# Kernel tuning notes

Hardware: AMD Instinct MI355X
Metric: run time of the kernel (lower is better)

Reference implementation:

```python
import jax, jax.numpy as jnp
import numpy as np
import math

B, T, D = 2, 2048, 1024
H, NL, DF = 16, 6, 4096
HD = D // H
EPS = 1e-5

def layer_norm(x, w, b):
    mu = jnp.mean(x, axis=-1, keepdims=True)
    var = jnp.mean((x - mu) ** 2, axis=-1, keepdims=True)
    return (x - mu) * jax.lax.rsqrt(var + EPS) * w + b

def setup_inputs() -> dict:
    key = jax.random.key(0)
    ks = jax.random.split(key, 12)
    def w(k, shape, scale=0.02):
        return jax.random.normal(k, shape, dtype=jnp.float32) * scale
    inp = {
        'sequences': jax.random.normal(ks[0], (B, T, D), dtype=jnp.float32),
        'Wq': w(ks[1], (NL, D, D)), 'bq': jnp.zeros((NL, D), jnp.float32),
        'Wk': w(ks[2], (NL, D, D)), 'bk': jnp.zeros((NL, D), jnp.float32),
        'Wv': w(ks[3], (NL, D, D)), 'bv': jnp.zeros((NL, D), jnp.float32),
        'Wo': w(ks[4], (NL, D, D)), 'bo': jnp.zeros((NL, D), jnp.float32),
        'Wz': w(ks[5], (NL, D, D)), 'bz': jnp.zeros((NL, D), jnp.float32),
        'Wr': w(ks[6], (NL, D, D)), 'br': jnp.zeros((NL, D), jnp.float32),
        'W1': w(ks[7], (NL, D, DF)), 'b1': jnp.zeros((NL, DF), jnp.float32),
        'W2': w(ks[8], (NL, DF, D)), 'b2': jnp.zeros((NL, D), jnp.float32),
        'ln1_w': jnp.ones((NL, D), jnp.float32), 'ln1_b': jnp.zeros((NL, D), jnp.float32),
        'ln2_w': jnp.ones((NL, D), jnp.float32), 'ln2_b': jnp.zeros((NL, D), jnp.float32),
        'lnf_w': jnp.ones((D,), jnp.float32), 'lnf_b': jnp.zeros((D,), jnp.float32),
    }
    return inp

def reference(sequences, Wq, bq, Wk, bk, Wv, bv, Wo, bo, Wz, bz, Wr, br,
              W1, b1, W2, b2, ln1_w, ln1_b, ln2_w, ln2_b, lnf_w, lnf_b):
    scale = 1.0 / math.sqrt(HD)
    causal = jnp.tril(jnp.ones((T, T), dtype=bool))  # mask[L:L+T, :L+T] with L=0
    x = sequences
    src = x
    for i in range(NL):
        xn = layer_norm(x, ln1_w[i], ln1_b[i])
        # QKV -> [B, H, T, HD]
        q = (xn @ Wq[i] + bq[i]).reshape(B, T, H, HD).transpose(0, 2, 1, 3)
        k = (xn @ Wk[i] + bk[i]).reshape(B, T, H, HD).transpose(0, 2, 1, 3)
        v = (xn @ Wv[i] + bv[i]).reshape(B, T, H, HD).transpose(0, 2, 1, 3)
        att = jnp.einsum('bhqd,bhkd->bhqk', q, k) * scale
        att = jnp.where(causal, att, -jnp.inf)
        att = jax.nn.softmax(att, axis=-1)
        y = jnp.einsum('bhqk,bhkd->bhqd', att, v)
        y = y.transpose(0, 2, 1, 3).reshape(B, T, D)
        x_attn = y @ Wo[i] + bo[i]
        z = jax.nn.sigmoid(xn @ Wz[i] + bz[i])
        r = jax.nn.sigmoid(xn @ Wr[i] + br[i])
        h_tilde = jnp.tanh(r * x_attn)
        x = (1.0 - z) * x + z * h_tilde
        xm = layer_norm(x, ln2_w[i], ln2_b[i])
        mlp = jax.nn.gelu(xm @ W1[i] + b1[i], approximate=False) @ W2[i] + b2[i]
        x = (1.0 - z) * x + z * mlp
        x = x + src
    x = layer_norm(x, lnf_w, lnf_b)
    return x
```

## Files before the change

kernel.cpp:

```cpp
#include <hip/hip_runtime.h>
#include <hip/hip_bf16.h>
#include <math.h>

#define B_ 2
#define T_ 2048
#define D_ 1024
#define H_ 16
#define NL_ 6
#define DF_ 4096
#define HD_ 64
#define M_ (B_*T_)

typedef __bf16 bf16;
typedef __attribute__((ext_vector_type(8))) __bf16 bf16x8;
typedef __attribute__((ext_vector_type(4))) float f32x4;
typedef __attribute__((ext_vector_type(16))) float f32x16;
typedef __attribute__((ext_vector_type(4))) unsigned u32x4;

#define BAR() __builtin_amdgcn_s_barrier()
#define LGKM0() asm volatile("s_waitcnt lgkmcnt(0)" ::: "memory")
#define VMC(n) asm volatile("s_waitcnt vmcnt(" #n ")" ::: "memory")

__device__ __forceinline__ void gload_lds16(const void* g, void* l) {
    __builtin_amdgcn_global_load_lds((const __attribute__((address_space(1))) void*)g,
                                     (__attribute__((address_space(3))) void*)l, 16, 0, 0);
}

__device__ __forceinline__ unsigned pk2(float a, float b) {
    bf16 lo = (bf16)a, hb = (bf16)b;
    return (unsigned)__builtin_bit_cast(unsigned short, lo) |
           ((unsigned)__builtin_bit_cast(unsigned short, hb) << 16);
}

template<bool OUT_BF16>
__global__ __launch_bounds__(256) void ln_kernel(const float* __restrict__ x,
        const float* __restrict__ w, const float* __restrict__ b,
        void* __restrict__ out) {
    const int row = blockIdx.x;
    const int t = threadIdx.x;
    const float4 xv = *(const float4*)(x + (long)row * D_ + t * 4);
    float s  = xv.x + xv.y + xv.z + xv.w;
    float sq = xv.x*xv.x + xv.y*xv.y + xv.z*xv.z + xv.w*xv.w;
    #pragma unroll
    for (int m = 32; m; m >>= 1) { s += __shfl_xor(s, m); sq += __shfl_xor(sq, m); }
    __shared__ float red[8];
    const int wid = t >> 6, lid = t & 63;
    if (lid == 0) { red[wid] = s; red[wid + 4] = sq; }
    __syncthreads();
    s  = red[0] + red[1] + red[2] + red[3];
    sq = red[4] + red[5] + red[6] + red[7];
    const float mu   = s * (1.0f / D_);
    const float var  = sq * (1.0f / D_) - mu * mu;
    const float rstd = rsqrtf(var + 1e-5f);
    const float4 wv = *(const float4*)(w + t * 4);
    const float4 bv = *(const float4*)(b + t * 4);
    float o0 = (xv.x - mu) * rstd * wv.x + bv.x;
    float o1 = (xv.y - mu) * rstd * wv.y + bv.y;
    float o2 = (xv.z - mu) * rstd * wv.z + bv.z;
    float o3 = (xv.w - mu) * rstd * wv.w + bv.w;
    if (OUT_BF16) {
        bf16* o = (bf16*)out + (long)row * D_ + t * 4;
        o[0] = (bf16)o0; o[1] = (bf16)o1; o[2] = (bf16)o2; o[3] = (bf16)o3;
    } else {
        float* o = (float*)out + (long)row * D_ + t * 4;
        o[0] = o0; o[1] = o1; o[2] = o2; o[3] = o3;
    }
}

__global__ __launch_bounds__(256) void wconv_all(
        const float* __restrict__ Wq, const float* __restrict__ Wk,
        const float* __restrict__ Wv, const float* __restrict__ Wz,
        const float* __restrict__ Wr, const float* __restrict__ Wo,
        const float* __restrict__ W1, const float* __restrict__ W2,
        bf16* __restrict__ wt) {
    __shared__ float s[32][33];
    const int bid = blockIdx.x;
    const float* src; bf16* dst; int t, K, nlg;
    if (bid < 6144) {
        const int m = bid >> 10; t = bid & 1023; K = 1024; nlg = 5;
        switch (m) {
            case 0: src = Wq; dst = wt; break;
            case 1: src = Wk; dst = wt + (1u << 20); break;
            case 2: src = Wv; dst = wt + (2u << 20); break;
            case 3: src = Wz; dst = wt + (3u << 20); break;
            case 4: src = Wr; dst = wt + (4u << 20); break;
            default: src = Wo; dst = wt + (5u << 20); break;
        }
    } else if (bid < 10240) {
        t = bid - 6144; K = 1024; nlg = 7; src = W1; dst = wt + (6u << 20);
    } else {
        t = bid - 10240; K = 4096; nlg = 5; src = W2; dst = wt + (10u << 20);
    }
    const int N = 1 << (nlg + 5);
    const int k0 = (t >> nlg) * 32, n0 = (t & ((1 << nlg) - 1)) * 32;
    const int c = threadIdx.x & 31, r8 = threadIdx.x >> 5;
    #pragma unroll
    for (int it = 0; it < 4; it++)
        s[r8 + it*8][c] = src[(long)(k0 + r8 + it*8) * N + n0 + c];
    __syncthreads();
    #pragma unroll
    for (int it = 0; it < 4; it++)
        dst[(long)(n0 + r8 + it*8) * K + k0 + c] = (bf16)s[c][r8 + it*8];
}

#define MFMA16(a, b, c) __builtin_amdgcn_mfma_f32_16x16x32_bf16(a, b, c, 0, 0, 0)

__device__ __forceinline__ void gemm128_core(const bf16* __restrict__ A, const bf16* __restrict__ Bt,
        const int Ks, const int NT, const int m0, const int n0, char* lds, f32x4 (&acc)[4][4]) {
    const int tid = threadIdx.x;
    const int lane = tid & 63, w = tid >> 6;
    const int wm = w >> 1, wn = w & 1;
    const int cl = lane & 15, gl = lane >> 4;
    const int srow = lane >> 2;
    const int sxc = (((lane & 3) ^ (srow & 3)) << 3);
    const bf16* pa0 = A  + (size_t)(m0 + w * 32 + srow) * Ks + sxc;
    const bf16* pa1 = pa0 + (size_t)16 * Ks;
    const bf16* pb  = Bt + (size_t)(n0 + w * 16 + srow) * Ks + sxc;
    char* laA = lds + w * 2048;
    char* laB = lds + 32768 + w * 1024;

#define STG(KT, BUF) do { \
    gload_lds16(pa0 + (size_t)(KT) * 32, laA + (BUF) * 16384); \
    gload_lds16(pa1 + (size_t)(KT) * 32, laA + (BUF) * 16384 + 1024); \
    gload_lds16(pb  + (size_t)(KT) * 32, laB + (BUF) * 8192); } while (0)

    STG(0, 0); STG(1, 1);
    VMC(3);
    BAR();

    const int xo  = ((gl ^ (cl & 3)) << 4);
    const int rdA = (wm * 64 + cl) * 64 + xo;
    const int rdB = (wn * 64 + cl) * 64 + xo;

    for (int kt = 0; kt < NT; ++kt) {
        const int buf = kt & 1;
        const char* sA = lds + buf * 16384;
        const char* sB = lds + 32768 + buf * 8192;
        bf16x8 a[4], b[4];
        #pragma unroll
        for (int mi = 0; mi < 4; mi++) a[mi] = *(const bf16x8*)(sA + rdA + mi * 1024);
        #pragma unroll
        for (int ni = 0; ni < 4; ni++) b[ni] = *(const bf16x8*)(sB + rdB + ni * 1024);
        BAR(); LGKM0();
        __builtin_amdgcn_s_setprio(1);
        #pragma unroll
        for (int mi = 0; mi < 2; mi++)
            #pragma unroll
            for (int ni = 0; ni < 4; ni++)
                acc[mi][ni] = MFMA16(a[mi], b[ni], acc[mi][ni]);
        __builtin_amdgcn_s_setprio(0);
        BAR();
        if (kt + 2 < NT) STG(kt + 2, buf);
        __builtin_amdgcn_s_setprio(1);
        #pragma unroll
        for (int mi = 2; mi < 4; mi++)
            #pragma unroll
            for (int ni = 0; ni < 4; ni++)
                acc[mi][ni] = MFMA16(a[mi], b[ni], acc[mi][ni]);
        __builtin_amdgcn_s_setprio(0);
        if (kt + 2 < NT)      { VMC(3); }
        else if (kt + 1 < NT) { VMC(0); }
        BAR();
    }
#undef STG
}

__global__ __launch_bounds__(512, 4) void gemm5_k(const bf16* __restrict__ A, const bf16* __restrict__ Bt,
        const float* __restrict__ bq, const float* __restrict__ bk, const float* __restrict__ bvv,
        const float* __restrict__ bz, const float* __restrict__ br,
        bf16* __restrict__ oq, bf16* __restrict__ ok, bf16* __restrict__ ov,
        float* __restrict__ oz, float* __restrict__ orr) {
    __shared__ __align__(16) char lds[49152];
    int bid = blockIdx.x;
    bid = (bid & 7) * 80 + (bid >> 3);
    const int m0 = (bid / 40) * 256, n0 = (bid % 40) * 128;
    f32x4 acc[4][4];
    #pragma unroll
    for (int i = 0; i < 4; i++)
        #pragma unroll
        for (int j = 0; j < 4; j++) acc[i][j] = (f32x4){0.f, 0.f, 0.f, 0.f};
    gemm128_core(A, Bt, 1024, 32, m0, n0, lds, acc);
    const int tid = threadIdx.x, lane = tid & 63, w = tid >> 6;
    const int wm = w >> 1, wn = w & 1, cl = lane & 15, gl = lane >> 4;
    const int seg = n0 >> 10;
    const int lc0 = (n0 & 1023) + wn * 64;
    const float* bias; int mode; void* outp;
    switch (seg) {
        case 0:  bias = bq;  mode = 0; outp = oq;  break;
        case 1:  bias = bk;  mode = 0; outp = ok;  break;
        case 2:  bias = bvv; mode = 1; outp = ov;  break;
        case 3:  bias = bz;  mode = 2; outp = oz;  break;
        default: bias = br;  mode = 2; outp = orr; break;
    }
    #pragma unroll
    for (int mi = 0; mi < 4; mi++) {
        #pragma unroll
        for (int ni = 0; ni < 4; ni++) {
            const int lcol = lc0 + ni * 16 + cl;
            const float bv = bias[lcol];
            #pragma unroll
            for (int r = 0; r < 4; r++) {
                const int row = m0 + wm * 64 + mi * 16 + gl * 4 + r;
                const float v = acc[mi][ni][r] + bv;
                if (mode == 0) {
                    ((bf16*)outp)[(long)row * 1024 + lcol] = (bf16)v;
                } else if (mode == 1) {
                    ((bf16*)outp)[((long)(row >> 11) * 1024 + lcol) * T_ + (row & 2047)] = (bf16)v;
                } else {
                    ((float*)outp)[(long)row * 1024 + lcol] = 1.0f / (1.0f + __expf(-v));
                }
            }
        }
    }
}

__global__ __launch_bounds__(512, 4) void gemmG_k(const bf16* __restrict__ A, const bf16* __restrict__ Bt,
        const float* __restrict__ bias, bf16* __restrict__ out) {
    __shared__ __align__(16) char lds[49152];
    int bid = blockIdx.x;
    bid = (bid & 7) * 64 + (bid >> 3);
    const int m0 = (bid >> 5) * 256, n0 = (bid & 31) * 128;
    f32x4 acc[4][4];
    #pragma unroll
    for (int i = 0; i < 4; i++)
        #pragma unroll
        for (int j = 0; j < 4; j++) acc[i][j] = (f32x4){0.f, 0.f, 0.f, 0.f};
    gemm128_core(A, Bt, 1024, 32, m0, n0, lds, acc);
    const int tid = threadIdx.x, lane = tid & 63, w = tid >> 6;
    const int wm = w >> 1, wn = w & 1, cl = lane & 15, gl = lane >> 4;
    #pragma unroll
    for (int mi = 0; mi < 4; mi++) {
        #pragma unroll
        for (int ni = 0; ni < 4; ni++) {
            const int col = n0 + wn * 64 + ni * 16 + cl;
            const float bv = bias[col];
            #pragma unroll
            for (int r = 0; r < 4; r++) {
                const int row = m0 + wm * 64 + mi * 16 + gl * 4 + r;
                float v = acc[mi][ni][r] + bv;
                v = 0.5f * v * (1.0f + erff(v * 0.70710678118f));
                out[(long)row * DF_ + col] = (bf16)v;
            }
        }
    }
}

__global__ __launch_bounds__(512, 4) void gemmP_k(const bf16* __restrict__ A, const bf16* __restrict__ Bt,
        float* __restrict__ p0, float* __restrict__ p1, float* __restrict__ p2, float* __restrict__ p3) {
    __shared__ __align__(16) char lds[49152];
    int bid = blockIdx.x;
    bid = (bid & 7) * 64 + (bid >> 3);
    const int mt = bid >> 5, s = (bid >> 3) & 3, ntl = bid & 7;
    const int m0 = mt * 256, n0 = ntl * 128;
    f32x4 acc[4][4];
    #pragma unroll
    for (int i = 0; i < 4; i++)
        #pragma unroll
        for (int j = 0; j < 4; j++) acc[i][j] = (f32x4){0.f, 0.f, 0.f, 0.f};
    gemm128_core(A + s * 1024, Bt + s * 1024, 4096, 32, m0, n0, lds, acc);
    float* outp = (s == 0) ? p0 : (s == 1) ? p1 : (s == 2) ? p2 : p3;
    const int tid = threadIdx.x, lane = tid & 63, w = tid >> 6;
    const int wm = w >> 1, wn = w & 1, cl = lane & 15, gl = lane >> 4;
    #pragma unroll
    for (int mi = 0; mi < 4; mi++) {
        #pragma unroll
        for (int ni = 0; ni < 4; ni++) {
            const int col = n0 + wn * 64 + ni * 16 + cl;
            #pragma unroll
            for (int r = 0; r < 4; r++) {
                const int row = m0 + wm * 64 + mi * 16 + gl * 4 + r;
                outp[(long)row * 1024 + col] = acc[mi][ni][r];
            }
        }
    }
}

__global__ __launch_bounds__(256) void gemmWo_kernel(const bf16* __restrict__ A,
        const bf16* __restrict__ Bt, const float* __restrict__ bias,
        float* __restrict__ out) {
    __shared__ bf16 sA[128 * 32];
    __shared__ bf16 sB[128 * 32];
    const int tid = threadIdx.x;
    int bid = blockIdx.x;
    bid = (bid & 7) * 32 + (bid >> 3);
    const int m0 = (bid >> 3) * 128, n0 = (bid & 7) * 128;
    f32x4 acc[4][4];
    #pragma unroll
    for (int i = 0; i < 4; i++)
        #pragma unroll
        for (int j = 0; j < 4; j++) acc[i][j] = (f32x4){0.f, 0.f, 0.f, 0.f};
    const int lane = tid & 63, w = tid >> 6;
    const int wr = (w >> 1) * 64, wc = (w & 1) * 64;
    const int cl = lane & 15, gl = lane >> 4;
    const int srow = tid >> 2, skoff = (tid & 3) * 8;
    const bf16* ga = A  + (long)(m0 + srow) * D_ + skoff;
    const bf16* gb = Bt + (long)(n0 + srow) * D_ + skoff;
    char* sAc = (char*)sA;
    char* sBc = (char*)sB;
    const int wb = w * 1024;
    for (int k0 = 0; k0 < D_; k0 += 32) {
        if (k0) __syncthreads();
        gload_lds16(ga + k0,            sAc + wb);
        gload_lds16(ga + 64 * D_ + k0,  sAc + 4096 + wb);
        gload_lds16(gb + k0,            sBc + wb);
        gload_lds16(gb + 64 * D_ + k0,  sBc + 4096 + wb);
        __syncthreads();
        bf16x8 af[4], bfr[4];
        #pragma unroll
        for (int i = 0; i < 4; i++) af[i]  = *(const bf16x8*)(sA + (wr + i*16 + cl) * 32 + 8 * gl);
        #pragma unroll
        for (int j = 0; j < 4; j++) bfr[j] = *(const bf16x8*)(sB + (wc + j*16 + cl) * 32 + 8 * gl);
        #pragma unroll
        for (int i = 0; i < 4; i++)
            #pragma unroll
            for (int j = 0; j < 4; j++)
                acc[i][j] = MFMA16(af[i], bfr[j], acc[i][j]);
    }
    #pragma unroll
    for (int i = 0; i < 4; i++) {
        #pragma unroll
        for (int j = 0; j < 4; j++) {
            const int gcol = n0 + wc + j * 16 + cl;
            const float bv = bias[gcol];
            #pragma unroll
            for (int r = 0; r < 4; r++) {
                const int grow = m0 + wr + i * 16 + gl * 4 + r;
                out[(long)grow * D_ + gcol] = acc[i][j][r] + bv;
            }
        }
    }
}

#define LOADKV(K0,K1,K2,K3,V00,V01,V10,V11,KVB) do { \
    const long kro_ = (long)((KVB) + col) * D_ + 8 * hi; \
    K0 = *(const bf16x8*)(kB + kro_); \
    K1 = *(const bf16x8*)(kB + kro_ + 16); \
    K2 = *(const bf16x8*)(kB + kro_ + 32); \
    K3 = *(const bf16x8*)(kB + kro_ + 48); \
    const long vro_ = (long)col * T_ + (KVB) + 8 * hi; \
    V00 = *(const bf16x8*)(vB + vro_); \
    V10 = *(const bf16x8*)(vB + vro_ + 16); \
    V01 = *(const bf16x8*)(vB + vro_ + (long)32 * T_); \
    V11 = *(const bf16x8*)(vB + vro_ + (long)32 * T_ + 16); \
} while (0)

#define PROC(K0,K1,K2,K3,V00,V01,V10,V11,JJ) do { \
    f32x16 S; \
    _Pragma("unroll") for (int i_ = 0; i_ < 16; i_++) S[i_] = 0.f; \
    S = __builtin_amdgcn_mfma_f32_32x32x16_bf16(K0, qf0, S, 0, 0, 0); \
    S = __builtin_amdgcn_mfma_f32_32x32x16_bf16(K1, qf1, S, 0, 0, 0); \
    S = __builtin_amdgcn_mfma_f32_32x32x16_bf16(K2, qf2, S, 0, 0, 0); \
    S = __builtin_amdgcn_mfma_f32_32x32x16_bf16(K3, qf3, S, 0, 0, 0); \
    float p_[16]; \
    const bool dg_ = (JJ) == nt - 1; \
    _Pragma("unroll") for (int r_ = 0; r_ < 16; r_++) { \
        p_[r_] = S[r_] * 0.125f; \
        const int kvl_ = (r_ & 3) + 8 * (r_ >> 2) + 4 * hi; \
        if (dg_ && kvl_ > col) p_[r_] = -3.0e38f; \
    } \
    float tm_ = p_[0]; \
    _Pragma("unroll") for (int r_ = 1; r_ < 16; r_++) tm_ = fmaxf(tm_, p_[r_]); \
    tm_ = fmaxf(tm_, __shfl_xor(tm_, 32)); \
    const float mn_ = fmaxf(mrun, tm_); \
    const float al_ = __expf(mrun - mn_); \
    mrun = mn_; \
    float ts_ = 0.f; \
    _Pragma("unroll") for (int r_ = 0; r_ < 16; r_++) { p_[r_] = __expf(p_[r_] - mn_); ts_ += p_[r_]; } \
    ts_ += __shfl_xor(ts_, 32); \
    lrun = lrun * al_ + ts_; \
    _Pragma("unroll") for (int i_ = 0; i_ < 16; i_++) { Od0[i_] *= al_; Od1[i_] *= al_; } \
    const unsigned w0_ = pk2(p_[0],  p_[1]),  w1_ = pk2(p_[2],  p_[3]); \
    const unsigned w2_ = pk2(p_[4],  p_[5]),  w3_ = pk2(p_[6],  p_[7]); \
    const unsigned w4_ = pk2(p_[8],  p_[9]),  w5_ = pk2(p_[10], p_[11]); \
    const unsigned w6_ = pk2(p_[12], p_[13]), w7_ = pk2(p_[14], p_[15]); \
    const unsigned x0_ = __shfl_xor((int)w0_, 32), x1_ = __shfl_xor((int)w1_, 32); \
    const unsigned x2_ = __shfl_xor((int)w2_, 32), x3_ = __shfl_xor((int)w3_, 32); \
    const unsigned x4_ = __shfl_xor((int)w4_, 32), x5_ = __shfl_xor((int)w5_, 32); \
    const unsigned x6_ = __shfl_xor((int)w6_, 32), x7_ = __shfl_xor((int)w7_, 32); \
    const u32x4 c0_ = hi ? (u32x4){x2_, x3_, w2_, w3_} : (u32x4){w0_, w1_, x0_, x1_}; \
    const u32x4 c1_ = hi ? (u32x4){x6_, x7_, w6_, w7_} : (u32x4){w4_, w5_, x4_, x5_}; \
    const bf16x8 pb0_ = __builtin_bit_cast(bf16x8, c0_); \
    const bf16x8 pb1_ = __builtin_bit_cast(bf16x8, c1_); \
    Od0 = __builtin_amdgcn_mfma_f32_32x32x16_bf16(V00, pb0_, Od0, 0, 0, 0); \
    Od0 = __builtin_amdgcn_mfma_f32_32x32x16_bf16(V10, pb1_, Od0, 0, 0, 0); \
    Od1 = __builtin_amdgcn_mfma_f32_32x32x16_bf16(V01, pb0_, Od1, 0, 0, 0); \
    Od1 = __builtin_amdgcn_mfma_f32_32x32x16_bf16(V11, pb1_, Od1, 0, 0, 0); \
} while (0)

__global__ __launch_bounds__(128) void attn_kernel(const bf16* __restrict__ q,
        const bf16* __restrict__ k, const bf16* __restrict__ vT,
        bf16* __restrict__ y) {
    const int tid = threadIdx.x, wid = tid >> 6, lane = tid & 63;
    const int col = lane & 31, hi = lane >> 5;
    const int bid = blockIdx.x;
    const int xcd = bid & 7, idx = bid >> 3;
    const int bh = xcd + 8 * (idx & 3);
    const int g = idx >> 2;
    const int qt = wid ? (63 - g) : g;
    const int qb = qt * 32;
    const int b = bh >> 4, h = bh & 15;

    const bf16* qB = q  + (long)b * T_ * D_ + h * HD_;
    const bf16* kB = k  + (long)b * T_ * D_ + h * HD_;
    const bf16* vB = vT + (long)b * D_ * T_ + (long)h * HD_ * T_;

    bf16x8 qf0, qf1, qf2, qf3;
    {
        const long qo = (long)(qb + col) * D_ + 8 * hi;
        qf0 = *(const bf16x8*)(qB + qo);
        qf1 = *(const bf16x8*)(qB + qo + 16);
        qf2 = *(const bf16x8*)(qB + qo + 32);
        qf3 = *(const bf16x8*)(qB + qo + 48);
    }

    f32x16 Od0, Od1;
    #pragma unroll
    for (int i = 0; i < 16; i++) { Od0[i] = 0.f; Od1[i] = 0.f; }
    float mrun = -INFINITY, lrun = 0.f;

    bf16x8 ka0, ka1, ka2, ka3, va00, va01, va10, va11;
    bf16x8 kb0, kb1, kb2, kb3, vb00, vb01, vb10, vb11;
    const int nt = qt + 1;

    int jj = 0;
    LOADKV(ka0, ka1, ka2, ka3, va00, va01, va10, va11, 0);
    while (true) {
        if (jj + 1 < nt) LOADKV(kb0, kb1, kb2, kb3, vb00, vb01, vb10, vb11, (jj + 1) * 32);
        PROC(ka0, ka1, ka2, ka3, va00, va01, va10, va11, jj);
        if (++jj >= nt) break;
        if (jj + 1 < nt) LOADKV(ka0, ka1, ka2, ka3, va00, va01, va10, va11, (jj + 1) * 32);
        PROC(kb0, kb1, kb2, kb3, vb00, vb01, vb10, vb11, jj);
        if (++jj >= nt) break;
    }

    const float inv = 1.0f / lrun;
    bf16* yr = y + (long)(b * T_ + qb + col) * D_ + h * HD_;
    #pragma unroll
    for (int rg = 0; rg < 4; rg++) {
        const int d0 = 8 * rg + 4 * hi;
        uint2 s0 = { pk2(Od0[4*rg] * inv, Od0[4*rg+1] * inv), pk2(Od0[4*rg+2] * inv, Od0[4*rg+3] * inv) };
        *(uint2*)(yr + d0) = s0;
        uint2 s1 = { pk2(Od1[4*rg] * inv, Od1[4*rg+1] * inv), pk2(Od1[4*rg+2] * inv, Od1[4*rg+3] * inv) };
        *(uint2*)(yr + 32 + d0) = s1;
    }
}

__global__ __launch_bounds__(256) void gate1_kernel(float* __restrict__ x,
        const float* __restrict__ z, const float* __restrict__ r,
        const float* __restrict__ xa) {
    const long i = ((long)blockIdx.x * 256 + threadIdx.x) * 4;
    float4 xv = *(const float4*)(x + i);
    const float4 zv = *(const float4*)(z + i);
    const float4 rv = *(const float4*)(r + i);
    const float4 av = *(const float4*)(xa + i);
    xv.x = (1.f - zv.x) * xv.x + zv.x * tanhf(rv.x * av.x);
    xv.y = (1.f - zv.y) * xv.y + zv.y * tanhf(rv.y * av.y);
    xv.z = (1.f - zv.z) * xv.z + zv.z * tanhf(rv.z * av.z);
    xv.w = (1.f - zv.w) * xv.w + zv.w * tanhf(rv.w * av.w);
    *(float4*)(x + i) = xv;
}

__global__ __launch_bounds__(256) void gate2_kernel(float* __restrict__ x,
        const float* __restrict__ z,
        const float* __restrict__ p0, const float* __restrict__ p1,
        const float* __restrict__ p2, const float* __restrict__ p3,
        const float* __restrict__ src, const float* __restrict__ b2) {
    const long i = ((long)blockIdx.x * 256 + threadIdx.x) * 4;
    float4 xv = *(const float4*)(x + i);
    const float4 zv = *(const float4*)(z + i);
    const float4 a0 = *(const float4*)(p0 + i);
    const float4 a1 = *(const float4*)(p1 + i);
    const float4 a2 = *(const float4*)(p2 + i);
    const float4 a3 = *(const float4*)(p3 + i);
    const float4 sv = *(const float4*)(src + i);
    const float4 bb = *(const float4*)(b2 + (i & 1023));
    const float mx = a0.x + a1.x + a2.x + a3.x + bb.x;
    const float my = a0.y + a1.y + a2.y + a3.y + bb.y;
    const float mz = a0.z + a1.z + a2.z + a3.z + bb.z;
    const float mw = a0.w + a1.w + a2.w + a3.w + bb.w;
    xv.x = (1.f - zv.x) * xv.x + zv.x * mx + sv.x;
    xv.y = (1.f - zv.y) * xv.y + zv.y * my + sv.y;
    xv.z = (1.f - zv.z) * xv.z + zv.z * mz + sv.z;
    xv.w = (1.f - zv.w) * xv.w + zv.w * mw + sv.w;
    *(float4*)(x + i) = xv;
}

extern "C" void kernel_launch(void* const* d_in, const int* in_sizes, int n_in,
                              void* d_out, int out_size, void* d_ws, size_t ws_size,
                              hipStream_t stream) {
    const float* seq   = (const float*)d_in[0];
    const float* Wq    = (const float*)d_in[1];  const float* bq = (const float*)d_in[2];
    const float* Wk    = (const float*)d_in[3];  const float* bk = (const float*)d_in[4];
    const float* Wv    = (const float*)d_in[5];  const float* bv = (const float*)d_in[6];
    const float* Wo    = (const float*)d_in[7];  const float* bo = (const float*)d_in[8];
    const float* Wz    = (const float*)d_in[9];  const float* bz = (const float*)d_in[10];
    const float* Wr    = (const float*)d_in[11]; const float* br = (const float*)d_in[12];
    const float* W1    = (const float*)d_in[13]; const float* b1 = (const float*)d_in[14];
    const float* W2    = (const float*)d_in[15]; const float* b2 = (const float*)d_in[16];
    const float* ln1w  = (const float*)d_in[17]; const float* ln1b = (const float*)d_in[18];
    const float* ln2w  = (const float*)d_in[19]; const float* ln2b = (const float*)d_in[20];
    const float* lnfw  = (const float*)d_in[21]; const float* lnfb = (const float*)d_in[22];

    char* ws = (char*)d_ws;
    float* x   = (float*)(ws);
    float* z   = (float*)(ws + ((size_t)16 << 20));
    float* r   = (float*)(ws + ((size_t)32 << 20));
    float* xa  = (float*)(ws + ((size_t)48 << 20));
    bf16*  xn  = (bf16*)(ws + ((size_t)64 << 20));
    bf16*  qb_ = (bf16*)(ws + ((size_t)72 << 20));
    bf16*  kb_ = (bf16*)(ws + ((size_t)80 << 20));
    bf16*  vtb = (bf16*)(ws + ((size_t)88 << 20));
    bf16*  yb  = (bf16*)(ws + ((size_t)96 << 20));
    bf16*  h1  = (bf16*)(ws + ((size_t)104 << 20));
    bf16*  wt  = (bf16*)(ws + ((size_t)136 << 20));
    float* pt2 = (float*)(ws + ((size_t)172 << 20));
    float* pt3 = (float*)(ws + ((size_t)188 << 20));

    bf16* wto = wt + (5u << 20);
    bf16* wt1 = wt + (6u << 20);
    bf16* wt2 = wt + (10u << 20);

    hipMemcpyAsync(x, seq, (size_t)M_ * D_ * 4, hipMemcpyDeviceToDevice, stream);

    for (int i = 0; i < NL_; i++) {
        const long dd = (long)i * D_ * D_;
        wconv_all<<<14336, 256, 0, stream>>>(Wq + dd, Wk + dd, Wv + dd, Wz + dd,
                                             Wr + dd, Wo + dd,
                                             W1 + (long)i * D_ * DF_,
                                             W2 + (long)i * DF_ * D_, wt);
        ln_kernel<true><<<M_, 256, 0, stream>>>(x, ln1w + i * D_, ln1b + i * D_, xn);
        gemm5_k<<<640, 512, 0, stream>>>(xn, wt,
                bq + i * D_, bk + i * D_, bv + i * D_, bz + i * D_, br + i * D_,
                qb_, kb_, vtb, z, r);
        attn_kernel<<<1024, 128, 0, stream>>>(qb_, kb_, vtb, yb);
        gemmWo_kernel<<<256, 256, 0, stream>>>(yb, wto, bo + i * D_, xa);
        gate1_kernel<<<(M_ * D_) / 1024, 256, 0, stream>>>(x, z, r, xa);
        ln_kernel<true><<<M_, 256, 0, stream>>>(x, ln2w + i * D_, ln2b + i * D_, xn);
        gemmG_k<<<512, 512, 0, stream>>>(xn, wt1, b1 + i * DF_, h1);
        gemmP_k<<<512, 512, 0, stream>>>(h1, wt2, xa, r, pt2, pt3);
        gate2_kernel<<<(M_ * D_) / 1024, 256, 0, stream>>>(x, z, xa, r, pt2, pt3, seq, b2 + i * D_);
    }
    ln_kernel<false><<<M_, 256, 0, stream>>>(x, lnfw, lnfb, d_out);
}
```

Before: 1.933 ms.

## Share K/V tiles across four waves via LDS in flash attention

The attention kernel now runs four waves per block, each handling one of four consecutive 32-row query tiles. K/V tiles of 64 keys are staged into swizzled, double-buffered LDS with global_load_lds, so one load is shared by all four waves instead of each wave reading K/V from global memory on its own. It also folds the 1/sqrt(d) scale into the Q projection epilogue and skips the rescale of the running output unless the max grows by more than 8. The cost is two block barriers per step and idle waves on the diagonal tail. Skipping the rescale lets unnormalised exponentials reach up to about e^8 before normalisation.

```diff
diff --git a/kernel.cpp b/kernel.cpp
--- a/kernel.cpp
+++ b/kernel.cpp
@@ -104,6 +104,7 @@
 }
 
 #define MFMA16(a, b, c) __builtin_amdgcn_mfma_f32_16x16x32_bf16(a, b, c, 0, 0, 0)
+#define MFMA32(a, b, c) __builtin_amdgcn_mfma_f32_32x32x16_bf16(a, b, c, 0, 0, 0)
 
 __device__ __forceinline__ void gemm128_core(const bf16* __restrict__ A, const bf16* __restrict__ Bt,
         const int Ks, const int NT, const int m0, const int n0, char* lds, f32x4 (&acc)[4][4]) {
@@ -192,6 +193,7 @@
         case 3:  bias = bz;  mode = 2; outp = oz;  break;
         default: bias = br;  mode = 2; outp = orr; break;
     }
+    const float scl = (seg == 0) ? 0.125f : 1.0f;
     #pragma unroll
     for (int mi = 0; mi < 4; mi++) {
         #pragma unroll
@@ -201,7 +203,7 @@
             #pragma unroll
             for (int r = 0; r < 4; r++) {
                 const int row = m0 + wm * 64 + mi * 16 + gl * 4 + r;
-                const float v = acc[mi][ni][r] + bv;
+                const float v = (acc[mi][ni][r] + bv) * scl;
                 if (mode == 0) {
                     ((bf16*)outp)[(long)row * 1024 + lcol] = (bf16)v;
                 } else if (mode == 1) {
@@ -331,86 +333,51 @@
     }
 }
 
-#define LOADKV(K0,K1,K2,K3,V00,V01,V10,V11,KVB) do { \
-    const long kro_ = (long)((KVB) + col) * D_ + 8 * hi; \
-    K0 = *(const bf16x8*)(kB + kro_); \
-    K1 = *(const bf16x8*)(kB + kro_ + 16); \
-    K2 = *(const bf16x8*)(kB + kro_ + 32); \
-    K3 = *(const bf16x8*)(kB + kro_ + 48); \
-    const long vro_ = (long)col * T_ + (KVB) + 8 * hi; \
-    V00 = *(const bf16x8*)(vB + vro_); \
-    V10 = *(const bf16x8*)(vB + vro_ + 16); \
-    V01 = *(const bf16x8*)(vB + vro_ + (long)32 * T_); \
-    V11 = *(const bf16x8*)(vB + vro_ + (long)32 * T_ + 16); \
-} while (0)
-
-#define PROC(K0,K1,K2,K3,V00,V01,V10,V11,JJ) do { \
-    f32x16 S; \
-    _Pragma("unroll") for (int i_ = 0; i_ < 16; i_++) S[i_] = 0.f; \
-    S = __builtin_amdgcn_mfma_f32_32x32x16_bf16(K0, qf0, S, 0, 0, 0); \
-    S = __builtin_amdgcn_mfma_f32_32x32x16_bf16(K1, qf1, S, 0, 0, 0); \
-    S = __builtin_amdgcn_mfma_f32_32x32x16_bf16(K2, qf2, S, 0, 0, 0); \
-    S = __builtin_amdgcn_mfma_f32_32x32x16_bf16(K3, qf3, S, 0, 0, 0); \
-    float p_[16]; \
-    const bool dg_ = (JJ) == nt - 1; \
-    _Pragma("unroll") for (int r_ = 0; r_ < 16; r_++) { \
-        p_[r_] = S[r_] * 0.125f; \
-        const int kvl_ = (r_ & 3) + 8 * (r_ >> 2) + 4 * hi; \
-        if (dg_ && kvl_ > col) p_[r_] = -3.0e38f; \
-    } \
-    float tm_ = p_[0]; \
-    _Pragma("unroll") for (int r_ = 1; r_ < 16; r_++) tm_ = fmaxf(tm_, p_[r_]); \
-    tm_ = fmaxf(tm_, __shfl_xor(tm_, 32)); \
-    const float mn_ = fmaxf(mrun, tm_); \
-    const float al_ = __expf(mrun - mn_); \
-    mrun = mn_; \
-    float ts_ = 0.f; \
-    _Pragma("unroll") for (int r_ = 0; r_ < 16; r_++) { p_[r_] = __expf(p_[r_] - mn_); ts_ += p_[r_]; } \
-    ts_ += __shfl_xor(ts_, 32); \
-    lrun = lrun * al_ + ts_; \
-    _Pragma("unroll") for (int i_ = 0; i_ < 16; i_++) { Od0[i_] *= al_; Od1[i_] *= al_; } \
-    const unsigned w0_ = pk2(p_[0],  p_[1]),  w1_ = pk2(p_[2],  p_[3]); \
-    const unsigned w2_ = pk2(p_[4],  p_[5]),  w3_ = pk2(p_[6],  p_[7]); \
-    const unsigned w4_ = pk2(p_[8],  p_[9]),  w5_ = pk2(p_[10], p_[11]); \
-    const unsigned w6_ = pk2(p_[12], p_[13]), w7_ = pk2(p_[14], p_[15]); \
-    const unsigned x0_ = __shfl_xor((int)w0_, 32), x1_ = __shfl_xor((int)w1_, 32); \
-    const unsigned x2_ = __shfl_xor((int)w2_, 32), x3_ = __shfl_xor((int)w3_, 32); \
-    const unsigned x4_ = __shfl_xor((int)w4_, 32), x5_ = __shfl_xor((int)w5_, 32); \
-    const unsigned x6_ = __shfl_xor((int)w6_, 32), x7_ = __shfl_xor((int)w7_, 32); \
-    const u32x4 c0_ = hi ? (u32x4){x2_, x3_, w2_, w3_} : (u32x4){w0_, w1_, x0_, x1_}; \
-    const u32x4 c1_ = hi ? (u32x4){x6_, x7_, w6_, w7_} : (u32x4){w4_, w5_, x4_, x5_}; \
-    const bf16x8 pb0_ = __builtin_bit_cast(bf16x8, c0_); \
-    const bf16x8 pb1_ = __builtin_bit_cast(bf16x8, c1_); \
-    Od0 = __builtin_amdgcn_mfma_f32_32x32x16_bf16(V00, pb0_, Od0, 0, 0, 0); \
-    Od0 = __builtin_amdgcn_mfma_f32_32x32x16_bf16(V10, pb1_, Od0, 0, 0, 0); \
-    Od1 = __builtin_amdgcn_mfma_f32_32x32x16_bf16(V01, pb0_, Od1, 0, 0, 0); \
-    Od1 = __builtin_amdgcn_mfma_f32_32x32x16_bf16(V11, pb1_, Od1, 0, 0, 0); \
-} while (0)
-
-__global__ __launch_bounds__(128) void attn_kernel(const bf16* __restrict__ q,
+__global__ __launch_bounds__(256, 2) void attn_kernel(const bf16* __restrict__ q,
         const bf16* __restrict__ k, const bf16* __restrict__ vT,
         bf16* __restrict__ y) {
+    __shared__ __align__(16) char lds[32768];
     const int tid = threadIdx.x, wid = tid >> 6, lane = tid & 63;
     const int col = lane & 31, hi = lane >> 5;
     const int bid = blockIdx.x;
     const int xcd = bid & 7, idx = bid >> 3;
     const int bh = xcd + 8 * (idx & 3);
-    const int g = idx >> 2;
-    const int qt = wid ? (63 - g) : g;
+    const int sg = idx >> 2;
+    const int g = (sg & 1) ? (sg >> 1) : (15 - (sg >> 1));
+    const int qt = 4 * g + wid;
     const int qb = qt * 32;
     const int b = bh >> 4, h = bh & 15;
-
-    const bf16* qB = q  + (long)b * T_ * D_ + h * HD_;
-    const bf16* kB = k  + (long)b * T_ * D_ + h * HD_;
-    const bf16* vB = vT + (long)b * D_ * T_ + (long)h * HD_ * T_;
+    const int NP = 2 * g + 2;
+    const int nt64 = (qt >> 1) + 1;
+
+    const bf16* qB = q  + (size_t)b * T_ * D_ + h * HD_;
+    const bf16* kB = k  + (size_t)b * T_ * D_ + h * HD_;
+    const bf16* vB = vT + (size_t)b * D_ * T_ + (size_t)h * HD_ * T_;
+
+    const int sr = wid * 8 + (lane >> 3);
+    const int sc = lane & 7;
+    const bf16* kS0 = kB + (size_t)sr * D_ + 8 * (sc ^ (sr & 7));
+    const bf16* kS1 = kS0 + (size_t)32 * D_;
+    const bf16* vS0 = vB + (size_t)sr * T_ + 8 * (sc ^ (sr & 7));
+    const bf16* vS1 = vS0 + (size_t)32 * T_;
+    char* dK = lds + wid * 1024;
+    char* dV = lds + 16384 + wid * 1024;
+
+#define ASTG(J, BUF) do { \
+    const size_t ko_ = (size_t)(J) * 64 * D_; \
+    const size_t vo_ = (size_t)(J) * 64; \
+    gload_lds16(kS0 + ko_, dK + (BUF) * 8192); \
+    gload_lds16(kS1 + ko_, dK + (BUF) * 8192 + 4096); \
+    gload_lds16(vS0 + vo_, dV + (BUF) * 8192); \
+    gload_lds16(vS1 + vo_, dV + (BUF) * 8192 + 4096); } while (0)
 
     bf16x8 qf0, qf1, qf2, qf3;
     {
-        const long qo = (long)(qb + col) * D_ + 8 * hi;
-        qf0 = *(const bf16x8*)(qB + qo);
-        qf1 = *(const bf16x8*)(qB + qo + 16);
-        qf2 = *(const bf16x8*)(qB + qo + 32);
-        qf3 = *(const bf16x8*)(qB + qo + 48);
+        const bf16* qp = qB + (size_t)(qb + col) * D_ + 8 * hi;
+        qf0 = *(const bf16x8*)(qp);
+        qf1 = *(const bf16x8*)(qp + 16);
+        qf2 = *(const bf16x8*)(qp + 32);
+        qf3 = *(const bf16x8*)(qp + 48);
     }
 
     f32x16 Od0, Od1;
@@ -418,23 +385,92 @@
     for (int i = 0; i < 16; i++) { Od0[i] = 0.f; Od1[i] = 0.f; }
     float mrun = -INFINITY, lrun = 0.f;
 
-    bf16x8 ka0, ka1, ka2, ka3, va00, va01, va10, va11;
-    bf16x8 kb0, kb1, kb2, kb3, vb00, vb01, vb10, vb11;
-    const int nt = qt + 1;
-
-    int jj = 0;
-    LOADKV(ka0, ka1, ka2, ka3, va00, va01, va10, va11, 0);
-    while (true) {
-        if (jj + 1 < nt) LOADKV(kb0, kb1, kb2, kb3, vb00, vb01, vb10, vb11, (jj + 1) * 32);
-        PROC(ka0, ka1, ka2, ka3, va00, va01, va10, va11, jj);
-        if (++jj >= nt) break;
-        if (jj + 1 < nt) LOADKV(ka0, ka1, ka2, ka3, va00, va01, va10, va11, (jj + 1) * 32);
-        PROC(kb0, kb1, kb2, kb3, vb00, vb01, vb10, vb11, jj);
-        if (++jj >= nt) break;
+    ASTG(0, 0);
+    ASTG(1, 1);
+    VMC(4);
+    BAR();
+
+    const int swz = col & 7;
+    for (int j = 0; j < NP; ++j) {
+        const int buf = j & 1;
+        if (j < nt64) {
+            const char* bK = lds + buf * 8192;
+            const char* bV = lds + 16384 + buf * 8192;
+            bf16x8 kf0[4], kf1[4], vf0[4], vf1[4];
+            #pragma unroll
+            for (int cs = 0; cs < 4; cs++) {
+                const int ch = ((hi + 2 * cs) ^ swz) * 16;
+                kf0[cs] = *(const bf16x8*)(bK + col * 128 + ch);
+                kf1[cs] = *(const bf16x8*)(bK + (col + 32) * 128 + ch);
+                vf0[cs] = *(const bf16x8*)(bV + col * 128 + ch);
+                vf1[cs] = *(const bf16x8*)(bV + (col + 32) * 128 + ch);
+            }
+            f32x16 S0, S1;
+            #pragma unroll
+            for (int i = 0; i < 16; i++) { S0[i] = 0.f; S1[i] = 0.f; }
+            S0 = MFMA32(kf0[0], qf0, S0); S0 = MFMA32(kf0[1], qf1, S0);
+            S0 = MFMA32(kf0[2], qf2, S0); S0 = MFMA32(kf0[3], qf3, S0);
+            S1 = MFMA32(kf1[0], qf0, S1); S1 = MFMA32(kf1[1], qf1, S1);
+            S1 = MFMA32(kf1[2], qf2, S1); S1 = MFMA32(kf1[3], qf3, S1);
+            float p[32];
+            #pragma unroll
+            for (int r = 0; r < 16; r++) { p[r] = S0[r]; p[16 + r] = S1[r]; }
+            if (j == nt64 - 1) {
+                const int qr = qb + col;
+                #pragma unroll
+                for (int r = 0; r < 32; r++) {
+                    const int kvl = 64 * j + 32 * (r >> 4)
+                                  + (r & 3) + 8 * ((r & 15) >> 2) + 4 * hi;
+                    if (kvl > qr) p[r] = -3.0e38f;
+                }
+            }
+            float tm = p[0];
+            #pragma unroll
+            for (int r = 1; r < 32; r++) tm = fmaxf(tm, p[r]);
+            tm = fmaxf(tm, __shfl_xor(tm, 32));
+            if (!__all(tm <= mrun + 8.f)) {
+                const float mn = fmaxf(mrun, tm);
+                const float al = __expf(mrun - mn);
+                lrun *= al;
+                #pragma unroll
+                for (int i = 0; i < 16; i++) { Od0[i] *= al; Od1[i] *= al; }
+                mrun = mn;
+            }
+            float ts = 0.f;
+            #pragma unroll
+            for (int r = 0; r < 32; r++) { p[r] = __expf(p[r] - mrun); ts += p[r]; }
+            ts += __shfl_xor(ts, 32);
+            lrun += ts;
+            bf16x8 pbf[4];
+            #pragma unroll
+            for (int t = 0; t < 2; t++) {
+                const unsigned pw0 = pk2(p[16*t+0],  p[16*t+1]),  pw1 = pk2(p[16*t+2],  p[16*t+3]);
+                const unsigned pw2 = pk2(p[16*t+4],  p[16*t+5]),  pw3 = pk2(p[16*t+6],  p[16*t+7]);
+                const unsigned pw4 = pk2(p[16*t+8],  p[16*t+9]),  pw5 = pk2(p[16*t+10], p[16*t+11]);
+                const unsigned pw6 = pk2(p[16*t+12], p[16*t+13]), pw7 = pk2(p[16*t+14], p[16*t+15]);
+                const unsigned px0 = __shfl_xor((int)pw0, 32), px1 = __shfl_xor((int)pw1, 32);
+                const unsigned px2 = __shfl_xor((int)pw2, 32), px3 = __shfl_xor((int)pw3, 32);
+                const unsigned px4 = __shfl_xor((int)pw4, 32), px5 = __shfl_xor((int)pw5, 32);
+                const unsigned px6 = __shfl_xor((int)pw6, 32), px7 = __shfl_xor((int)pw7, 32);
+                const u32x4 c0 = hi ? (u32x4){px2, px3, pw2, pw3} : (u32x4){pw0, pw1, px0, px1};
+                const u32x4 c1 = hi ? (u32x4){px6, px7, pw6, pw7} : (u32x4){pw4, pw5, px4, px5};
+                pbf[2*t]   = __builtin_bit_cast(bf16x8, c0);
+                pbf[2*t+1] = __builtin_bit_cast(bf16x8, c1);
+            }
+            #pragma unroll
+            for (int f = 0; f < 4; f++) {
+                Od0 = MFMA32(vf0[f], pbf[f], Od0);
+                Od1 = MFMA32(vf1[f], pbf[f], Od1);
+            }
+        }
+        BAR();
+        if (j + 2 < NP) { ASTG(j + 2, buf); VMC(4); }
+        else            { VMC(0); }
+        BAR();
     }
 
     const float inv = 1.0f / lrun;
-    bf16* yr = y + (long)(b * T_ + qb + col) * D_ + h * HD_;
+    bf16* yr = y + (size_t)(b * T_ + qb + col) * D_ + h * HD_;
     #pragma unroll
     for (int rg = 0; rg < 4; rg++) {
         const int d0 = 8 * rg + 4 * hi;
@@ -443,6 +479,7 @@
         uint2 s1 = { pk2(Od1[4*rg] * inv, Od1[4*rg+1] * inv), pk2(Od1[4*rg+2] * inv, Od1[4*rg+3] * inv) };
         *(uint2*)(yr + 32 + d0) = s1;
     }
+#undef ASTG
 }
 
 __global__ __launch_bounds__(256) void gate1_kernel(float* __restrict__ x,
@@ -532,7 +569,7 @@
         gemm5_k<<<640, 512, 0, stream>>>(xn, wt,
                 bq + i * D_, bk + i * D_, bv + i * D_, bz + i * D_, br + i * D_,
                 qb_, kb_, vtb, z, r);
-        attn_kernel<<<1024, 128, 0, stream>>>(qb_, kb_, vtb, yb);
+        attn_kernel<<<512, 256, 0, stream>>>(qb_, kb_, vtb, yb);
         gemmWo_kernel<<<256, 256, 0, stream>>>(yb, wto, bo + i * D_, xa);
         gate1_kernel<<<(M_ * D_) / 1024, 256, 0, stream>>>(x, z, r, xa);
         ln_kernel<true><<<M_, 256, 0, stream>>>(x, ln2w + i * D_, ln2b + i * D_, xn);
```

After: 1.795 ms. -7.1%, faster.
